# Optimization experiments

Hardware: AMD Instinct MI355X
Metric: run time of the kernel (lower is better)

The kernel has to match this reference:

```python
import jax, jax.numpy as jnp
import numpy as np
from jax import lax
from jax.scipy.stats import norm

K = 2            # top-k
NUM_EXPERTS = 4
NOISE_EPS = 0.01
LOSS_COEF = 0.01


def conv3x3(x, w):
    # x: [B,Cin,H,W], w: [Cout,Cin,3,3] -> [B,Cout,H,W]
    return lax.conv_general_dilated(x, w, (1, 1), 'SAME',
                                    dimension_numbers=('NCHW', 'OIHW', 'NCHW'))


def setup_inputs() -> dict:
    key = jax.random.key(0)
    ks = jax.random.split(key, 16)
    B, C, H, W = 16, 3, 256, 256
    FC = 2 * C                      # freq channels = 6
    HID = 64
    D = H * W * C                   # flattened gating dim = 196608
    f32 = jnp.float32
    inp = {
        'x':   jax.random.normal(ks[0], (B, C, H, W), f32),
        'ref': jax.random.normal(ks[1], (B, C, H, W), f32),
        'noise': jax.random.normal(ks[2], (B, NUM_EXPERTS), f32),
        'mod_w1': (jax.random.normal(ks[3], (FC, 2 * FC), f32) * 0.1),
        'mod_b1': jnp.zeros((FC,), f32),
        'mod_w2': (jax.random.normal(ks[4], (FC, FC), f32) * 0.1),
        'mod_b2': jnp.zeros((FC,), f32),
        'enh_w': (jax.random.normal(ks[5], (FC, FC), f32) * 0.1),
        'enh_b': jnp.zeros((FC,), f32),
        'fre_prompt': (jax.random.normal(ks[6], (FC, H, W // 2 + 1), f32) * 0.1),
        'w_gate':  (jax.random.normal(ks[7], (D, NUM_EXPERTS), f32) * 0.002),
        'w_noise': (jax.random.normal(ks[8], (D, NUM_EXPERTS), f32) * 0.002),
        'ew1': (jax.random.normal(ks[9],  (NUM_EXPERTS, HID, C, 3, 3), f32) * 0.05),
        'eb1': jnp.zeros((NUM_EXPERTS, HID), f32),
        'ew2': (jax.random.normal(ks[10], (NUM_EXPERTS, 1, HID, 3, 3), f32) * 0.05),
        'eb2': jnp.zeros((NUM_EXPERTS, 1), f32),
    }
    return inp


def _cv_squared(v):
    # torch .var() is unbiased (ddof=1)
    return jnp.var(v, ddof=1) / (jnp.mean(v) ** 2 + 1e-10)


def _forward(x, ref, noise, mod_w1, mod_b1, mod_w2, mod_b2, enh_w, enh_b,
             fre_prompt, w_gate, w_noise, ew1, eb1, ew2, eb2):
    B, C, H, W = x.shape

    # ---- frequency_prompt(ref) ----
    fft = jnp.fft.rfft2(ref, norm='ortho')                    # [B,C,H,W//2+1]
    freq = jnp.concatenate([fft.real, fft.imag], axis=1)      # [B,2C,H,Wf]
    # Adaptive avg/max pool to (H, W//2+1) are identities at native size
    pooled = jnp.concatenate([freq, freq], axis=1)            # [B,4C,H,Wf]
    m = jnp.einsum('oi,bihw->bohw', mod_w1, pooled) + mod_b1[:, None, None]
    m = jax.nn.relu(m)
    m = jnp.einsum('oi,bihw->bohw', mod_w2, m) + mod_b2[:, None, None]
    enh = m * fre_prompt[None]                                # [B,2C,H,Wf]
    enh = jax.nn.relu(jnp.einsum('oi,bihw->bohw', enh_w, enh) + enh_b[:, None, None])
    re, im = jnp.split(enh, 2, axis=1)
    spatial = jnp.fft.irfft2(re + 1j * im, s=(H, W), norm='ortho')  # [B,C,H,W]
    prompt = jax.nn.softmax(spatial.mean(axis=(2, 3), keepdims=True), axis=1)  # [B,C,1,1]

    # ---- noisy top-k gating ----
    x_ds = (x * prompt + x).reshape(B, -1)                    # [B, H*W*C]
    clean_logits = x_ds @ w_gate                              # [B,E]
    noise_stddev = jax.nn.softplus(x_ds @ w_noise) + NOISE_EPS
    noisy_logits = clean_logits + noise * noise_stddev
    top_vals, top_idx = lax.top_k(noisy_logits, K + 1)        # sorted desc, [B,K+1]
    tk_gates = jax.nn.softmax(top_vals[:, :K], axis=1)        # [B,K]
    gates = jnp.zeros_like(noisy_logits).at[
        jnp.arange(B)[:, None], top_idx[:, :K]].set(tk_gates)  # [B,E]

    # load = prob each expert's noisy logit lands in top-k
    thr_in = top_vals[:, K:K + 1]
    thr_out = top_vals[:, K - 1:K]
    is_in = noisy_logits > thr_in
    prob = jnp.where(is_in,
                     norm.cdf((clean_logits - thr_in) / noise_stddev),
                     norm.cdf((clean_logits - thr_out) / noise_stddev))
    load = prob.sum(0)
    importance = gates.sum(0)
    loss = (_cv_squared(importance) + _cv_squared(load)) * LOSS_COEF

    # ---- expert dispatch/combine (== weighted sum; gates are 0 off top-k) ----
    y = jnp.zeros((B, ew2.shape[1], H, W), x.dtype)
    for e in range(NUM_EXPERTS):
        h = jax.nn.relu(conv3x3(x, ew1[e]) + eb1[e][None, :, None, None])
        o = conv3x3(h, ew2[e]) + eb2[e][None, :, None, None]
        y = y + gates[:, e][:, None, None, None] * o
    return y, loss


def reference(x, ref, noise, mod_w1, mod_b1, mod_w2, mod_b2, enh_w, enh_b,
              fre_prompt, w_gate, w_noise, ew1, eb1, ew2, eb2):
    return _forward(x, ref, noise, mod_w1, mod_b1, mod_w2, mod_b2, enh_w, enh_b,
                    fre_prompt, w_gate, w_noise, ew1, eb1, ew2, eb2)
```

## Files before the change

kernel.cpp:

```cpp
#include <hip/hip_runtime.h>
#include <hip/hip_bf16.h>
#include <math.h>

#define WS_GATE 192
#define WS_GNP  256
#define WS_W1F  25088
#define WS_W2F  29184

typedef float    float4v __attribute__((ext_vector_type(4)));
typedef short    short8v __attribute__((ext_vector_type(8)));
typedef _Float16 half8v  __attribute__((ext_vector_type(8)));

union Q4 { uint4 q; short8v s; half8v h; };

__device__ __forceinline__ unsigned short bf16b(float f) {
    unsigned u = __builtin_bit_cast(unsigned, f);
    u = (u + 0x7FFFu + ((u >> 16) & 1u)) >> 16;
    return (unsigned short)u;
}

__device__ __forceinline__ unsigned pkbf16(float a, float b) {
#if __has_builtin(__builtin_amdgcn_cvt_pk_bf16_f32)
    return __builtin_bit_cast(unsigned, __builtin_amdgcn_cvt_pk_bf16_f32(a, b));
#else
    return (unsigned)bf16b(a) | ((unsigned)bf16b(b) << 16);
#endif
}

__device__ __forceinline__ unsigned pkf16(float a, float b) {
#if __has_builtin(__builtin_amdgcn_cvt_pkrtz)
    return __builtin_bit_cast(unsigned, __builtin_amdgcn_cvt_pkrtz(a, b));
#else
    union { _Float16 h[2]; unsigned u; } p;
    p.h[0] = (_Float16)a; p.h[1] = (_Float16)b;
    return p.u;
#endif
}

__global__ void k_aux(const float* __restrict__ ref, const float* __restrict__ x,
                      const float* __restrict__ wg,  const float* __restrict__ wn,
                      const float* __restrict__ ew1, const float* __restrict__ ew2,
                      float* __restrict__ ws) {
    __shared__ float sh[4][16][8];
    int blk = blockIdx.x, t = threadIdx.x;

    if (blk < 192) {
        int bc = blk >> 2, chunk = blk & 3;
        const float4* p4 = (const float4*)(ref + (size_t)bc*65536 + (size_t)chunk*16384);
        float acc = 0.f;
        #pragma unroll
        for (int i = 0; i < 16; ++i) { float4 v = p4[i*256 + t]; acc += v.x + v.y + v.z + v.w; }
        #pragma unroll
        for (int m = 1; m <= 32; m <<= 1) acc += __shfl_xor(acc, m);
        if ((t & 63) == 0) sh[0][0][t >> 6] = acc;
        __syncthreads();
        if (t == 0) ws[bc*4 + chunk] = sh[0][0][0] + sh[0][0][1] + sh[0][0][2] + sh[0][0][3];
        return;
    }
    if (blk < 384) {
        int r = blk - 192;
        int c = r >> 6, chunk = r & 63;
        int lane = t & 63, wv = t >> 6;
        int hw0 = chunk*1024 + t*4;
        const float4* wg4 = (const float4*)wg;
        const float4* wn4 = (const float4*)wn;
        const float4* x4  = (const float4*)x;
        float4 G[4], Nw[4];
        #pragma unroll
        for (int i = 0; i < 4; ++i) {
            G[i]  = wg4[c*65536 + hw0 + i];
            Nw[i] = wn4[c*65536 + hw0 + i];
        }
        for (int b = 0; b < 16; ++b) {
            float4 xv = x4[(b*3 + c)*16384 + chunk*256 + t];
            float xs[4] = {xv.x, xv.y, xv.z, xv.w};
            float aG[4] = {0,0,0,0}, aN[4] = {0,0,0,0};
            #pragma unroll
            for (int i = 0; i < 4; ++i) {
                aG[0] += xs[i]*G[i].x;  aG[1] += xs[i]*G[i].y;
                aG[2] += xs[i]*G[i].z;  aG[3] += xs[i]*G[i].w;
                aN[0] += xs[i]*Nw[i].x; aN[1] += xs[i]*Nw[i].y;
                aN[2] += xs[i]*Nw[i].z; aN[3] += xs[i]*Nw[i].w;
            }
            #pragma unroll
            for (int m = 1; m <= 32; m <<= 1) {
                #pragma unroll
                for (int e = 0; e < 4; ++e) {
                    aG[e] += __shfl_xor(aG[e], m);
                    aN[e] += __shfl_xor(aN[e], m);
                }
            }
            if (lane == 0) {
                #pragma unroll
                for (int e = 0; e < 4; ++e) { sh[wv][b][e] = aG[e]; sh[wv][b][4+e] = aN[e]; }
            }
        }
        __syncthreads();
        if (t < 128) {
            int b = t >> 3, s = t & 7;
            float v = sh[0][b][s] + sh[1][b][s] + sh[2][b][s] + sh[3][b][s];
            ws[WS_GNP + ((size_t)(c*64 + chunk)*16 + b)*8 + s] = v;
        }
        return;
    }
    uint4* w1f = (uint4*)(ws + WS_W1F);
    for (int i = t; i < 1024; i += 256) {
        int mm = i & 15, r = i >> 4, qq = r & 3, r2 = r >> 2, f = r2 & 3, e = r2 >> 2;
        const float* w1 = ew1 + e*1728 + (f*16 + mm)*27 + qq*8;
        int navail = 27 - qq*8;
        float v[8];
        #pragma unroll
        for (int j = 0; j < 8; ++j) v[j] = (j < navail) ? w1[j] : 0.f;
        uint4 q;
        q.x = pkbf16(v[0], v[1]); q.y = pkbf16(v[2], v[3]);
        q.z = pkbf16(v[4], v[5]); q.w = pkbf16(v[6], v[7]);
        w1f[i] = q;
    }
    uint4* w2f = (uint4*)(ws + WS_W2F);
    for (int i = t; i < 512; i += 256) {
        int qq = i & 3, r = i >> 2, ks = r & 1, r2 = r >> 1, mm = r2 & 15, e = r2 >> 4;
        uint4 q = make_uint4(0, 0, 0, 0);
        if (mm < 9) {
            float v[8];
            #pragma unroll
            for (int j = 0; j < 8; ++j) v[j] = ew2[e*576 + (ks*32 + qq*8 + j)*9 + mm];
            q.x = pkf16(v[0], v[1]); q.y = pkf16(v[2], v[3]);
            q.z = pkf16(v[4], v[5]); q.w = pkf16(v[6], v[7]);
        }
        w2f[i] = q;
    }
}

__global__ void k_gating(const float* __restrict__ noise,
                         const float* __restrict__ mw1, const float* __restrict__ mb1,
                         const float* __restrict__ mw2, const float* __restrict__ mb2,
                         const float* __restrict__ enw, const float* __restrict__ enb,
                         const float* __restrict__ fp,
                         float* __restrict__ ws, float* __restrict__ out) {
    __shared__ float GN2[48*8];
    __shared__ float gL[16][4], pL[16][4], cvs[2];
    int t = threadIdx.x;
    #pragma unroll
    for (int u = 0; u < 3; ++u) {
        int idx = t*3 + u;
        int bc = idx >> 3, s = idx & 7;
        int b = bc / 3, c = bc - b*3;
        float v = 0.f;
        for (int ch = 0; ch < 64; ++ch)
            v += ws[WS_GNP + ((size_t)(c*64 + ch)*16 + b)*8 + s];
        GN2[bc*8 + s] = v;
    }
    __syncthreads();
    if (t < 16) {
        int b = t;
        float sc[3];
        for (int c = 0; c < 3; ++c) {
            int bc = b*3 + c;
            sc[c] = (ws[bc*4] + ws[bc*4+1] + ws[bc*4+2] + ws[bc*4+3]) * (1.f/256.f);
        }
        float pooled[12];
        for (int i = 0; i < 12; ++i) { int r = i % 6; pooled[i] = (r < 3) ? sc[r] : 0.f; }
        float m1[6];
        for (int o = 0; o < 6; ++o) {
            float a = mb1[o];
            for (int i = 0; i < 12; ++i) a += mw1[o*12 + i] * pooled[i];
            m1[o] = fmaxf(a, 0.f);
        }
        float m2[6];
        for (int o = 0; o < 6; ++o) {
            float a = mb2[o];
            for (int i = 0; i < 6; ++i) a += mw2[o*6 + i] * m1[i];
            m2[o] = a * fp[(size_t)o * 33024];
        }
        float dc[3];
        for (int o = 0; o < 3; ++o) {
            float a = enb[o];
            for (int i = 0; i < 6; ++i) a += enw[o*6 + i] * m2[i];
            dc[o] = fmaxf(a, 0.f) * (1.f/256.f);
        }
        float mx = fmaxf(dc[0], fmaxf(dc[1], dc[2]));
        float e0 = expf(dc[0]-mx), e1 = expf(dc[1]-mx), e2 = expf(dc[2]-mx);
        float inv = 1.f / (e0 + e1 + e2);
        float pc[3] = { e0*inv + 1.f, e1*inv + 1.f, e2*inv + 1.f };
        float cl[4], sg[4], nz[4];
        for (int e = 0; e < 4; ++e) {
            float a = 0.f, nr = 0.f;
            for (int c = 0; c < 3; ++c) {
                a  += pc[c] * GN2[(b*3 + c)*8 + e];
                nr += pc[c] * GN2[(b*3 + c)*8 + 4 + e];
            }
            cl[e] = a;
            float sp = (nr > 20.f) ? nr : log1pf(expf(nr));
            sg[e] = sp + 0.01f;
            nz[e] = a + noise[b*4 + e] * sg[e];
        }
        int i0 = 0; float v0 = nz[0];
        for (int e = 1; e < 4; ++e) if (nz[e] > v0) { v0 = nz[e]; i0 = e; }
        int i1 = -1; float v1 = -3.4e38f;
        for (int e = 0; e < 4; ++e) if (e != i0 && nz[e] > v1) { v1 = nz[e]; i1 = e; }
        float v2 = -3.4e38f;
        for (int e = 0; e < 4; ++e) if (e != i0 && e != i1 && nz[e] > v2) v2 = nz[e];
        float ex = expf(v1 - v0), den = 1.f + ex;
        float gate[4] = {0.f, 0.f, 0.f, 0.f};
        gate[i0] = 1.f/den; gate[i1] = ex/den;
        for (int e = 0; e < 4; ++e) {
            ws[WS_GATE + b*4 + e] = gate[e];
            gL[b][e] = gate[e];
            float thr = (nz[e] > v2) ? v2 : v1;
            pL[b][e] = 0.5f * (1.f + erff((cl[e] - thr) / sg[e] * 0.70710678118f));
        }
    }
    __syncthreads();
    if (t < 2) {
        float v[4];
        for (int e = 0; e < 4; ++e) {
            float s = 0.f;
            for (int b = 0; b < 16; ++b) s += (t == 0) ? gL[b][e] : pL[b][e];
            v[e] = s;
        }
        float mean = 0.25f * (v[0] + v[1] + v[2] + v[3]);
        float var = 0.f;
        for (int e = 0; e < 4; ++e) { float d = v[e] - mean; var += d*d; }
        var *= (1.f/3.f);
        cvs[t] = var / (mean*mean + 1e-10f);
    }
    __syncthreads();
    if (t == 0) out[1048576] = (cvs[0] + cvs[1]) * 0.01f;
}

__global__ __launch_bounds__(256, 3)
void k_experts(const float* __restrict__ x,  const float* __restrict__ eb1,
               const float* __restrict__ eb2, const float* __restrict__ ws,
               float* __restrict__ out) {
    __shared__ __align__(16) uint4 s_hid[324*8];
    __shared__ __align__(16) char  s_mix[5904];
    float*    in_s = (float*)s_mix;
    _Float16* s_T  = (_Float16*)s_mix;

    int t = threadIdx.x;
    int b = blockIdx.x >> 8, tile = blockIdx.x & 255;
    int ty0 = (tile >> 4) * 16, tx0 = (tile & 15) * 16;
    const float* xb = x + (size_t)b * 196608;

    for (int i = t; i < 1200; i += 256) {
        int ci = i / 400, r = i - ci*400, iy = r / 20, ix = r - iy*20;
        int gy = ty0 - 2 + iy, gx = tx0 - 2 + ix;
        float v = 0.f;
        if ((unsigned)gy < 256u && (unsigned)gx < 256u) v = xb[ci*65536 + gy*256 + gx];
        in_s[i] = v;
    }
    __syncthreads();

    int lane = t & 63, wv = t >> 6;
    int qq = lane >> 4, mm = lane & 15;
    int oy = t >> 4, ox = t & 15;

    int offj[8];
    #pragma unroll
    for (int j = 0; j < 8; ++j) {
        int k = qq*8 + j;
        if (k < 27) { int ci = k/9, r = k - ci*9, kh = r/3, kw = r - kh*3;
                      offj[j] = ci*400 + kh*20 + kw; }
        else offj[j] = -1;
    }

    Q4 bfr[6];
    #pragma unroll
    for (int i = 0; i < 6; ++i) {
        int gidx = wv + i*4;
        if (gidx >= 21) break;
        int p = gidx*16 + mm;
        int py = p/18, px = p - py*18;
        int base = (p < 324) ? (py*20 + px) : 0;
        float v[8];
        #pragma unroll
        for (int j = 0; j < 8; ++j)
            v[j] = (offj[j] >= 0) ? in_s[base + offj[j]] : 0.f;
        bfr[i].q.x = pkbf16(v[0], v[1]); bfr[i].q.y = pkbf16(v[2], v[3]);
        bfr[i].q.z = pkbf16(v[4], v[5]); bfr[i].q.w = pkbf16(v[6], v[7]);
    }

    bool interior = (ty0 > 0) && (ty0 < 240) && (tx0 > 0) && (tx0 < 240);
    const float4 gates = *(const float4*)(ws + WS_GATE + b*4);
    float gv[4] = {gates.x, gates.y, gates.z, gates.w};
    const uint4* w1f = (const uint4*)(ws + WS_W1F);
    const uint4* w2f = (const uint4*)(ws + WS_W2F);
    float accY = 0.f;

    for (int e = 0; e < 4; ++e) {
        float g = gv[e];
        if (g == 0.f) continue;

        Q4 bw0, bw1;
        bw0.q = w2f[((e*16 + mm)*2 + 0)*4 + qq];
        bw1.q = w2f[((e*16 + mm)*2 + 1)*4 + qq];

        Q4 af[4];
        float4v cinit[4];
        #pragma unroll
        for (int f = 0; f < 4; ++f) {
            af[f].q = w1f[((e*4 + f)*4 + qq)*16 + mm];
            float4 bb = *(const float4*)(eb1 + e*64 + f*16 + qq*4);
            cinit[f] = (float4v){bb.x, bb.y, bb.z, bb.w};
        }

        #pragma unroll
        for (int i = 0; i < 6; ++i) {
            int gidx = wv + i*4;
            if (gidx >= 21) break;
            int p = gidx*16 + mm;
            bool valid = p < 324;
            float msk = 1.f;
            if (!interior) {
                int py = p/18, px = p - py*18;
                int gy = ty0 - 1 + py, gx = tx0 - 1 + px;
                msk = (((unsigned)gy < 256u) && ((unsigned)gx < 256u)) ? 1.f : 0.f;
            }
            #pragma unroll
            for (int f = 0; f < 4; ++f) {
                float4v d = __builtin_amdgcn_mfma_f32_16x16x32_bf16(
                    af[f].s, bfr[i].s, cinit[f], 0, 0, 0);
                if (valid) {
                    float h0 = fmaxf(d[0], 0.f);
                    float h1 = fmaxf(d[1], 0.f);
                    float h2 = fmaxf(d[2], 0.f);
                    float h3 = fmaxf(d[3], 0.f);
                    if (!interior) { h0 *= msk; h1 *= msk; h2 *= msk; h3 *= msk; }
                    uint2 pk = make_uint2(pkf16(h0, h1), pkf16(h2, h3));
                    int ch0 = f*16 + qq*4;
                    int hchunk = ch0 >> 3, hsel = (ch0 >> 2) & 1;
                    ((uint2*)&s_hid[p*8 + ((hchunk + p) & 7)])[hsel] = pk;
                }
            }
        }
        __syncthreads();

        for (int gi = wv; gi < 21; gi += 4) {
            int base = gi*16; if (base > 308) base = 308;
            int p = base + mm;
            Q4 a0, a1;
            a0.q = s_hid[p*8 + ((qq + p) & 7)];
            a1.q = s_hid[p*8 + ((4 + qq + p) & 7)];
            float4v d = __builtin_amdgcn_mfma_f32_16x16x32_f16(
                a0.h, bw0.h, (float4v){0.f,0.f,0.f,0.f}, 0, 0, 0);
            d = __builtin_amdgcn_mfma_f32_16x16x32_f16(a1.h, bw1.h, d, 0, 0, 0);
            if (mm < 9) {
                *(uint2*)&s_T[mm*328 + base + qq*4] =
                    make_uint2(pkf16(d[0], d[1]), pkf16(d[2], d[3]));
            }
        }
        __syncthreads();

        float oacc = 0.f;
        #pragma unroll
        for (int kh = 0; kh < 3; ++kh) {
            #pragma unroll
            for (int kw = 0; kw < 3; ++kw)
                oacc += (float)s_T[(kh*3 + kw)*328 + (oy + kh)*18 + ox + kw];
        }
        accY += g * (oacc + eb2[e]);
    }
    out[(size_t)b*65536 + (ty0 + oy)*256 + tx0 + ox] = accY;
}

extern "C" void kernel_launch(void* const* d_in, const int* in_sizes, int n_in,
                              void* d_out, int out_size, void* d_ws, size_t ws_size,
                              hipStream_t stream) {
    (void)in_sizes; (void)n_in; (void)out_size; (void)ws_size;
    const float* x     = (const float*)d_in[0];
    const float* ref   = (const float*)d_in[1];
    const float* noise = (const float*)d_in[2];
    const float* mw1   = (const float*)d_in[3];
    const float* mb1   = (const float*)d_in[4];
    const float* mw2   = (const float*)d_in[5];
    const float* mb2   = (const float*)d_in[6];
    const float* enw   = (const float*)d_in[7];
    const float* enb   = (const float*)d_in[8];
    const float* fp    = (const float*)d_in[9];
    const float* wg    = (const float*)d_in[10];
    const float* wn    = (const float*)d_in[11];
    const float* ew1   = (const float*)d_in[12];
    const float* eb1   = (const float*)d_in[13];
    const float* ew2   = (const float*)d_in[14];
    const float* eb2   = (const float*)d_in[15];
    float* out = (float*)d_out;
    float* ws  = (float*)d_ws;

    k_aux    <<<385, 256, 0, stream>>>(ref, x, wg, wn, ew1, ew2, ws);
    k_gating <<<1, 128, 0, stream>>>(noise, mw1, mb1, mw2, mb2, enw, enb, fp, ws, out);
    k_experts<<<4096, 256, 0, stream>>>(x, eb1, eb2, ws, out);
}
```

Baseline: 187.7 us.

## Split hidden channels into two halves to halve LDS and raise occupancy

The 64-channel hidden activation tile is now produced and consumed in two 32-channel halves. Second-conv partial results are accumulated in registers across both halves. This halves the s_hid shared buffer, which lets the launch bound rise from 3 to 4 blocks per SIMD. The cost is an extra pair of barriers per expert, six live accumulator registers across the halves, and more register pressure under the tighter bound.

```diff
diff --git a/kernel.cpp b/kernel.cpp
--- a/kernel.cpp
+++ b/kernel.cpp
@@ -228,11 +228,11 @@
     if (t == 0) out[1048576] = (cvs[0] + cvs[1]) * 0.01f;
 }
 
-__global__ __launch_bounds__(256, 3)
+__global__ __launch_bounds__(256, 4)
 void k_experts(const float* __restrict__ x,  const float* __restrict__ eb1,
                const float* __restrict__ eb2, const float* __restrict__ ws,
                float* __restrict__ out) {
-    __shared__ __align__(16) uint4 s_hid[324*8];
+    __shared__ __align__(16) uint4 s_hid[324*4];
     __shared__ __align__(16) char  s_mix[5904];
     float*    in_s = (float*)s_mix;
     _Float16* s_T  = (_Float16*)s_mix;
@@ -291,62 +291,75 @@
         float g = gv[e];
         if (g == 0.f) continue;
 
-        Q4 bw0, bw1;
-        bw0.q = w2f[((e*16 + mm)*2 + 0)*4 + qq];
-        bw1.q = w2f[((e*16 + mm)*2 + 1)*4 + qq];
-
-        Q4 af[4];
-        float4v cinit[4];
-        #pragma unroll
-        for (int f = 0; f < 4; ++f) {
-            af[f].q = w1f[((e*4 + f)*4 + qq)*16 + mm];
-            float4 bb = *(const float4*)(eb1 + e*64 + f*16 + qq*4);
-            cinit[f] = (float4v){bb.x, bb.y, bb.z, bb.w};
-        }
-
-        #pragma unroll
-        for (int i = 0; i < 6; ++i) {
-            int gidx = wv + i*4;
-            if (gidx >= 21) break;
-            int p = gidx*16 + mm;
-            bool valid = p < 324;
-            float msk = 1.f;
-            if (!interior) {
-                int py = p/18, px = p - py*18;
-                int gy = ty0 - 1 + py, gx = tx0 - 1 + px;
-                msk = (((unsigned)gy < 256u) && ((unsigned)gx < 256u)) ? 1.f : 0.f;
-            }
-            #pragma unroll
-            for (int f = 0; f < 4; ++f) {
-                float4v d = __builtin_amdgcn_mfma_f32_16x16x32_bf16(
-                    af[f].s, bfr[i].s, cinit[f], 0, 0, 0);
-                if (valid) {
-                    float h0 = fmaxf(d[0], 0.f);
-                    float h1 = fmaxf(d[1], 0.f);
-                    float h2 = fmaxf(d[2], 0.f);
-                    float h3 = fmaxf(d[3], 0.f);
-                    if (!interior) { h0 *= msk; h1 *= msk; h2 *= msk; h3 *= msk; }
-                    uint2 pk = make_uint2(pkf16(h0, h1), pkf16(h2, h3));
-                    int ch0 = f*16 + qq*4;
-                    int hchunk = ch0 >> 3, hsel = (ch0 >> 2) & 1;
-                    ((uint2*)&s_hid[p*8 + ((hchunk + p) & 7)])[hsel] = pk;
+        float4v tacc[6];
+        #pragma unroll
+        for (int i = 0; i < 6; ++i) tacc[i] = (float4v){0.f, 0.f, 0.f, 0.f};
+
+        #pragma unroll
+        for (int h = 0; h < 2; ++h) {
+            __syncthreads();
+
+            Q4 bw;
+            bw.q = w2f[((e*16 + mm)*2 + h)*4 + qq];
+            Q4 af[2];
+            float4v cinit[2];
+            #pragma unroll
+            for (int fh = 0; fh < 2; ++fh) {
+                int f = h*2 + fh;
+                af[fh].q = w1f[((e*4 + f)*4 + qq)*16 + mm];
+                float4 bb = *(const float4*)(eb1 + e*64 + f*16 + qq*4);
+                cinit[fh] = (float4v){bb.x, bb.y, bb.z, bb.w};
+            }
+
+            #pragma unroll
+            for (int i = 0; i < 6; ++i) {
+                int gidx = wv + i*4;
+                if (gidx >= 21) break;
+                int p = gidx*16 + mm;
+                bool valid = p < 324;
+                float msk = 1.f;
+                if (!interior) {
+                    int py = p/18, px = p - py*18;
+                    int gy = ty0 - 1 + py, gx = tx0 - 1 + px;
+                    msk = (((unsigned)gy < 256u) && ((unsigned)gx < 256u)) ? 1.f : 0.f;
                 }
-            }
-        }
-        __syncthreads();
-
-        for (int gi = wv; gi < 21; gi += 4) {
-            int base = gi*16; if (base > 308) base = 308;
-            int p = base + mm;
-            Q4 a0, a1;
-            a0.q = s_hid[p*8 + ((qq + p) & 7)];
-            a1.q = s_hid[p*8 + ((4 + qq + p) & 7)];
-            float4v d = __builtin_amdgcn_mfma_f32_16x16x32_f16(
-                a0.h, bw0.h, (float4v){0.f,0.f,0.f,0.f}, 0, 0, 0);
-            d = __builtin_amdgcn_mfma_f32_16x16x32_f16(a1.h, bw1.h, d, 0, 0, 0);
-            if (mm < 9) {
+                #pragma unroll
+                for (int fh = 0; fh < 2; ++fh) {
+                    float4v d = __builtin_amdgcn_mfma_f32_16x16x32_bf16(
+                        af[fh].s, bfr[i].s, cinit[fh], 0, 0, 0);
+                    if (valid) {
+                        float h0 = fmaxf(d[0], 0.f);
+                        float h1 = fmaxf(d[1], 0.f);
+                        float h2 = fmaxf(d[2], 0.f);
+                        float h3 = fmaxf(d[3], 0.f);
+                        if (!interior) { h0 *= msk; h1 *= msk; h2 *= msk; h3 *= msk; }
+                        uint2 pk = make_uint2(pkf16(h0, h1), pkf16(h2, h3));
+                        int ch0 = fh*16 + qq*4;
+                        int hchunk = ch0 >> 3, hsel = (ch0 >> 2) & 1;
+                        ((uint2*)&s_hid[p*4 + ((hchunk + p) & 3)])[hsel] = pk;
+                    }
+                }
+            }
+            __syncthreads();
+
+            int idx = 0;
+            for (int gi = wv; gi < 21; gi += 4, ++idx) {
+                int base = gi*16; if (base > 308) base = 308;
+                int p = base + mm;
+                Q4 a0;
+                a0.q = s_hid[p*4 + ((qq + p) & 3)];
+                tacc[idx] = __builtin_amdgcn_mfma_f32_16x16x32_f16(
+                    a0.h, bw.h, tacc[idx], 0, 0, 0);
+            }
+        }
+
+        if (mm < 9) {
+            int idx = 0;
+            for (int gi = wv; gi < 21; gi += 4, ++idx) {
+                int base = gi*16; if (base > 308) base = 308;
                 *(uint2*)&s_T[mm*328 + base + qq*4] =
-                    make_uint2(pkf16(d[0], d[1]), pkf16(d[2], d[3]));
+                    make_uint2(pkf16(tacc[idx][0], tacc[idx][1]),
+                               pkf16(tacc[idx][2], tacc[idx][3]));
             }
         }
         __syncthreads();
```

Measured after the change: 194.1 us. +3.4%, slower.
